# Kernel optimization log

Measured on AMD Instinct MI355X. Metric: run time of the kernel, lower is better.

## Reference

```python
import jax, jax.numpy as jnp
import numpy as np
import math

B, L, D = 4, 4096, 1024
M = 256  # num random features
EPS = 1e-06


def setup_inputs() -> dict:
    key = jax.random.key(0)
    kq, kk, kv, kp = jax.random.split(key, 4)
    Q = jax.random.normal(kq, (B, L, D), dtype=jnp.float32)
    K = jax.random.normal(kk, (B, L, D), dtype=jnp.float32)
    V = jax.random.normal(kv, (B, L, D), dtype=jnp.float32)
    # Gaussian random projection (ortho_features=False path): shape (num_features, d_model)
    projection = jax.random.normal(kp, (M, D), dtype=jnp.float32)
    return {"Q": Q, "K": K, "V": V, "projection": projection}


def reference(Q, K, V, projection):
    d_model = Q.shape[-1]
    m = projection.shape[0]
    inv_sqrt_d = 1.0 / math.sqrt(d_model)
    # random features: exp((x / sqrt(d)) @ P^T)
    rf_q = jnp.exp(jnp.einsum('bld,md->blm', Q * inv_sqrt_d, projection)) / math.sqrt(m)  # (B,L,M)
    rf_k = jnp.exp(jnp.einsum('bld,md->blm', K * inv_sqrt_d, projection))                 # (B,L,M)
    # linear attention: KV state and normalizer
    KV = jnp.einsum('blm,bld->bmd', rf_k, V)   # (B,M,D)
    Z = jnp.sum(rf_k, axis=1)                   # (B,M)
    out = jnp.einsum('blm,bmd->bld', rf_q, KV)  # (B,L,D)
    normalizer = jnp.einsum('blm,bm->bl', rf_q, Z) + EPS  # (B,L)
    return out / normalizer[..., None]
```

## Files before the change

kernel.cpp:

```cpp
#include <hip/hip_runtime.h>
#include <math.h>

#define NB 4
#define LL 4096
#define DD 1024
#define MM 256

typedef short s16x8 __attribute__((ext_vector_type(8)));
typedef short s16x4 __attribute__((ext_vector_type(4)));
typedef float fx4 __attribute__((ext_vector_type(4)));
typedef unsigned u32x2 __attribute__((ext_vector_type(2)));
typedef unsigned u32x4 __attribute__((ext_vector_type(4)));

__device__ __forceinline__ float b2f(short s) {
  union { unsigned u; float f; } v;
  v.u = ((unsigned)(unsigned short)s) << 16;
  return v.f;
}
__device__ __forceinline__ short f2b(float f) {
  union { float f; unsigned u; } v;
  v.f = f;
  unsigned r = (v.u + 0x7fffu + ((v.u >> 16) & 1u)) >> 16;
  return (short)(unsigned short)r;
}
__device__ __forceinline__ unsigned cvt2(float lo, float hi) {
  unsigned r;
  asm("v_cvt_pk_bf16_f32 %0, %1, %2" : "=v"(r) : "v"(lo), "v"(hi));
  return r;
}
__device__ __forceinline__ int keyf(int m) { return (m ^ (m >> 2)) & 3; }

typedef __attribute__((address_space(1))) const void* gas1_t;
typedef __attribute__((address_space(3))) void* las3_t;
#define GLL16(g, l) __builtin_amdgcn_global_load_lds((gas1_t)(const void*)(g), (las3_t)(void*)(l), 16, 0, 0)

__global__ __launch_bounds__(256) void k_cast(const float* __restrict__ in, short* __restrict__ out, int n4) {
  int i = blockIdx.x * 256 + threadIdx.x;
  if (i >= n4) return;
  float4 v = ((const float4*)in)[i];
  s16x4 s;
  s[0] = f2b(v.x); s[1] = f2b(v.y); s[2] = f2b(v.z); s[3] = f2b(v.w);
  ((s16x4*)out)[i] = s;
}

__global__ __launch_bounds__(256, 2) void k_qk(const float* __restrict__ Q, const float* __restrict__ K,
                                               const short* __restrict__ Pb,
                                               short* __restrict__ rfq, short* __restrict__ rfkT,
                                               float* __restrict__ Zz) {
  __shared__ short As[64 * 256];
  __shared__ short Bs[2][8192];
  int z = blockIdx.z, mode = z >> 2, b = z & 3;
  int l0 = blockIdx.x * 64;
  const float* X = mode ? K : Q;
  int tid = threadIdx.x, lane = tid & 63, w = tid >> 6;
  int m16 = lane & 15, kg = lane >> 4;

  int arow = tid >> 2, acol = (tid & 3) * 64;
  int akey = (arow & 7) << 4;
  char* Asb = (char*)As + arow * 512;

  fx4 acc[4][4] = {};

  for (int c = 0; c < 4; ++c) {
    if (c) __syncthreads();
    const float* Xc = X + ((size_t)b * LL + l0 + arow) * DD + c * 256 + acol;
    float4 pa[16];
    #pragma unroll
    for (int i = 0; i < 16; ++i) pa[i] = *(const float4*)(Xc + i * 4);
    #pragma unroll
    for (int j = 0; j < 4; ++j) {
      int fl = tid + j * 256, m = fl >> 2, ch = fl & 3;
      GLL16(Pb + (size_t)m * DD + c * 256 + (ch ^ keyf(m)) * 8, &Bs[0][fl * 8]);
    }
    #pragma unroll
    for (int i = 0; i < 8; ++i) {
      u32x4 v;
      v[0] = cvt2(pa[2 * i].x, pa[2 * i].y);
      v[1] = cvt2(pa[2 * i].z, pa[2 * i].w);
      v[2] = cvt2(pa[2 * i + 1].x, pa[2 * i + 1].y);
      v[3] = cvt2(pa[2 * i + 1].z, pa[2 * i + 1].w);
      int colb = (tid & 3) * 128 + i * 16;
      *(u32x4*)(Asb + (colb ^ akey)) = v;
    }
    __syncthreads();
    for (int s = 0; s < 8; ++s) {
      int buf = s & 1;
      if (s < 7) {
        #pragma unroll
        for (int j = 0; j < 4; ++j) {
          int fl = tid + j * 256, m = fl >> 2, ch = fl & 3;
          GLL16(Pb + (size_t)m * DD + c * 256 + (s + 1) * 32 + (ch ^ keyf(m)) * 8, &Bs[buf ^ 1][fl * 8]);
        }
      }
      s16x8 af[4], bf[4];
      int colb = s * 64 + kg * 16;
      #pragma unroll
      for (int mi = 0; mi < 4; ++mi) {
        int row = mi * 16 + m16;
        af[mi] = *(const s16x8*)((const char*)As + row * 512 + (colb ^ ((row & 7) << 4)));
      }
      #pragma unroll
      for (int ni = 0; ni < 4; ++ni) {
        int m = w * 64 + ni * 16 + m16;
        bf[ni] = *(const s16x8*)&Bs[buf][m * 32 + (kg ^ keyf(m)) * 8];
      }
      #pragma unroll
      for (int mi = 0; mi < 4; ++mi)
        #pragma unroll
        for (int ni = 0; ni < 4; ++ni)
          acc[mi][ni] = __builtin_amdgcn_mfma_f32_16x16x32_bf16(af[mi], bf[ni], acc[mi][ni], 0, 0, 0);
      if (s < 7) __syncthreads();
    }
  }

  if (mode == 0) {
    #pragma unroll
    for (int mi = 0; mi < 4; ++mi)
      #pragma unroll
      for (int ni = 0; ni < 4; ++ni) {
        int r0 = mi * 16 + (kg << 2);
        int c = w * 64 + ni * 16 + m16;
        #pragma unroll
        for (int u = 0; u < 4; ++u)
          rfq[((size_t)b * LL + l0 + r0 + u) * MM + c] = f2b(expf(acc[mi][ni][u] * 0.03125f) * 0.0625f);
      }
  } else {
    __syncthreads();
    short* T = (short*)Bs;
    float zp[4] = {0.f, 0.f, 0.f, 0.f};
    #pragma unroll
    for (int mi = 0; mi < 4; ++mi)
      #pragma unroll
      for (int ni = 0; ni < 4; ++ni) {
        int l = mi * 16 + (kg << 2);
        int m = w * 64 + ni * 16 + m16;
        int key = (m & 7) << 3;
        float e0 = expf(acc[mi][ni][0] * 0.03125f);
        float e1 = expf(acc[mi][ni][1] * 0.03125f);
        float e2 = expf(acc[mi][ni][2] * 0.03125f);
        float e3 = expf(acc[mi][ni][3] * 0.03125f);
        zp[ni] += e0 + e1 + e2 + e3;
        *(unsigned*)&T[m * 64 + (l ^ key)] = cvt2(e0, e1);
        *(unsigned*)&T[m * 64 + ((l ^ key) + 2)] = cvt2(e2, e3);
      }
    #pragma unroll
    for (int ni = 0; ni < 4; ++ni) {
      zp[ni] += __shfl_xor(zp[ni], 16);
      zp[ni] += __shfl_xor(zp[ni], 32);
    }
    if (kg == 0) {
      #pragma unroll
      for (int ni = 0; ni < 4; ++ni)
        atomicAdd(&Zz[b * MM + w * 64 + ni * 16 + m16], zp[ni]);
    }
    __syncthreads();
    int m = tid, mkey = (m & 7) << 3;
    short* dst = rfkT + ((size_t)b * MM + m) * LL + l0;
    #pragma unroll
    for (int j = 0; j < 8; ++j) {
      s16x8 v = *(const s16x8*)&T[m * 64 + ((j * 8) ^ mkey)];
      *(s16x8*)(dst + j * 8) = v;
    }
  }
}

__global__ __launch_bounds__(512) void k_kv(const float* __restrict__ V, const short* __restrict__ rfkT,
                                            float* __restrict__ KVp) {
  __shared__ float Vs[2][32 * 129];
  __shared__ short Ak[2][256 * 32];
  int d0 = blockIdx.x * 128, kc = blockIdx.y, b = blockIdx.z;
  int ls = kc * 512;
  int tid = threadIdx.x, lane = tid & 63, w = tid >> 6;
  int wm = w >> 1, wd = w & 1;
  int m16 = lane & 15, kg = lane >> 4;

  int vl = tid >> 4, vf = (tid & 15) * 8;
  const float* Vb = V + ((size_t)b * LL + ls + vl) * DD + d0 + vf;

  int am = tid >> 2, as = tid & 3;
  int acs = as ^ keyf(am);
  const short* AkS0 = rfkT + ((size_t)b * MM + am) * LL + ls + acs * 8;
  const short* AkS1 = rfkT + ((size_t)b * MM + am + 128) * LL + ls + acs * 8;

  fx4 acc[4][4] = {};
  float4 pv0, pv1;

  pv0 = *(const float4*)(Vb);
  pv1 = *(const float4*)(Vb + 4);
  GLL16(AkS0, &Ak[0][tid * 8]);
  GLL16(AkS1, &Ak[0][(tid + 512) * 8]);
  #pragma unroll
  for (int j = 0; j < 4; ++j) {
    Vs[0][vl * 129 + vf + j] = ((const float*)&pv0)[j];
    Vs[0][vl * 129 + vf + 4 + j] = ((const float*)&pv1)[j];
  }
  __syncthreads();

  for (int ch = 0; ch < 16; ++ch) {
    int cur = ch & 1, nxt = cur ^ 1;
    if (ch < 15) {
      int lo = (ch + 1) * 32;
      pv0 = *(const float4*)(Vb + (size_t)lo * DD);
      pv1 = *(const float4*)(Vb + (size_t)lo * DD + 4);
      GLL16(AkS0 + lo, &Ak[nxt][tid * 8]);
      GLL16(AkS1 + lo, &Ak[nxt][(tid + 512) * 8]);
    }
    s16x8 af[4];
    #pragma unroll
    for (int mi = 0; mi < 4; ++mi) {
      int m = wm * 64 + mi * 16 + m16;
      af[mi] = *(const s16x8*)&Ak[cur][m * 32 + ((kg ^ keyf(m)) * 8)];
    }
    #pragma unroll
    for (int ni = 0; ni < 4; ++ni) {
      int d = wd * 64 + ni * 16 + m16;
      const float* vs = &Vs[cur][kg * 8 * 129 + d];
      u32x4 bw;
      bw[0] = cvt2(vs[0], vs[129]);
      bw[1] = cvt2(vs[258], vs[387]);
      bw[2] = cvt2(vs[516], vs[645]);
      bw[3] = cvt2(vs[774], vs[903]);
      s16x8 bf = *(s16x8*)&bw;
      #pragma unroll
      for (int mi = 0; mi < 4; ++mi)
        acc[mi][ni] = __builtin_amdgcn_mfma_f32_16x16x32_bf16(af[mi], bf, acc[mi][ni], 0, 0, 0);
    }
    if (ch < 15) {
      #pragma unroll
      for (int j = 0; j < 4; ++j) {
        Vs[nxt][vl * 129 + vf + j] = ((const float*)&pv0)[j];
        Vs[nxt][vl * 129 + vf + 4 + j] = ((const float*)&pv1)[j];
      }
    }
    __syncthreads();
  }

  float* dst = KVp + (((size_t)kc * NB + b) * DD + d0) * MM;
  #pragma unroll
  for (int mi = 0; mi < 4; ++mi)
    #pragma unroll
    for (int ni = 0; ni < 4; ++ni) {
      int d = wd * 64 + ni * 16 + m16;
      int m = wm * 64 + mi * 16 + (kg << 2);
      *(float4*)(dst + (size_t)d * MM + m) = *(float4*)&acc[mi][ni];
    }
}

__global__ __launch_bounds__(256) void k_red(const float* __restrict__ KVp, float* __restrict__ KVTf) {
  int i = blockIdx.x * 256 + threadIdx.x;
  const float4* p = (const float4*)KVp;
  float4 s = p[i];
  #pragma unroll
  for (int k = 1; k < 8; ++k) {
    float4 v = p[i + k * 262144];
    s.x += v.x; s.y += v.y; s.z += v.z; s.w += v.w;
  }
  ((float4*)KVTf)[i] = s;
}

__global__ __launch_bounds__(512) void k_out(const short* __restrict__ rfq, const float* __restrict__ KVTf,
                                             const float* __restrict__ Zz, float* __restrict__ out) {
  __shared__ short Aq[2][8192];
  __shared__ short Bv[2][8192];
  __shared__ float zl[256];
  __shared__ float np[512];
  __shared__ float nf[128];
  int l0 = blockIdx.x * 128, d0 = blockIdx.y * 128, b = blockIdx.z;
  int tid = threadIdx.x, lane = tid & 63, w = tid >> 6;
  int wr = w >> 2, wc = w & 3;
  int brow = tid >> 2, bq = (tid & 3) * 16;
  int bkey = (brow & 7) << 3;
  const float* Kf = KVTf + ((size_t)b * DD + d0 + brow) * MM + bq;
  short* Bw0 = &Bv[0][brow * 64 + (bq ^ bkey)];
  short* Bw1 = &Bv[0][brow * 64 + ((bq + 8) ^ bkey)];
  const short* Ab = rfq + ((size_t)b * LL + l0) * MM;
  int f1 = tid + 512;
  int ar0 = tid >> 3, ac0 = tid & 7, ar1 = f1 >> 3, ac1 = f1 & 7;
  int nrow = tid & 127, nsub = tid >> 7;
  if (tid < 256) zl[tid] = Zz[b * MM + tid];
  fx4 acc[4][2] = {};
  float4 pb[4];
  float na = 0.f;

  #pragma unroll
  for (int i = 0; i < 4; ++i) pb[i] = *(const float4*)(Kf + i * 4);
  GLL16(Ab + (size_t)ar0 * MM + (ac0 ^ (ar0 & 7)) * 8, &Aq[0][tid * 8]);
  GLL16(Ab + (size_t)ar1 * MM + (ac1 ^ (ar1 & 7)) * 8, &Aq[0][f1 * 8]);
  {
    u32x2 v0, v1;
    v0[0] = cvt2(pb[0].x, pb[0].y); v0[1] = cvt2(pb[0].z, pb[0].w);
    v1[0] = cvt2(pb[1].x, pb[1].y); v1[1] = cvt2(pb[1].z, pb[1].w);
    *(u32x2*)Bw0 = v0;
    *(u32x2*)(Bw0 + 4) = v1;
    v0[0] = cvt2(pb[2].x, pb[2].y); v0[1] = cvt2(pb[2].z, pb[2].w);
    v1[0] = cvt2(pb[3].x, pb[3].y); v1[1] = cvt2(pb[3].z, pb[3].w);
    *(u32x2*)Bw1 = v0;
    *(u32x2*)(Bw1 + 4) = v1;
  }
  __syncthreads();

  for (int t = 0; t < 4; ++t) {
    int cur = t & 1, nxt = cur ^ 1;
    int m1 = ((t + 1) & 3) * 64;
    #pragma unroll
    for (int i = 0; i < 4; ++i) pb[i] = *(const float4*)(Kf + m1 + i * 4);
    GLL16(Ab + (size_t)ar0 * MM + m1 + (ac0 ^ (ar0 & 7)) * 8, &Aq[nxt][tid * 8]);
    GLL16(Ab + (size_t)ar1 * MM + m1 + (ac1 ^ (ar1 & 7)) * 8, &Aq[nxt][f1 * 8]);
    #pragma unroll
    for (int kk = 0; kk < 16; ++kk) {
      int k = nsub * 16 + kk;
      na += b2f(Aq[cur][nrow * 64 + (k ^ ((nrow & 7) << 3))]) * zl[t * 64 + k];
    }
    #pragma unroll
    for (int ks = 0; ks < 2; ++ks) {
      int kb = ks * 32 + (lane >> 4) * 8;
      s16x8 af[4], bf[2];
      #pragma unroll
      for (int mi = 0; mi < 4; ++mi) {
        int row = wr * 64 + mi * 16 + (lane & 15);
        af[mi] = *(const s16x8*)&Aq[cur][row * 64 + (kb ^ ((row & 7) << 3))];
      }
      #pragma unroll
      for (int ni = 0; ni < 2; ++ni) {
        int row = wc * 32 + ni * 16 + (lane & 15);
        bf[ni] = *(const s16x8*)&Bv[cur][row * 64 + (kb ^ ((row & 7) << 3))];
      }
      #pragma unroll
      for (int mi = 0; mi < 4; ++mi)
        #pragma unroll
        for (int ni = 0; ni < 2; ++ni)
          acc[mi][ni] = __builtin_amdgcn_mfma_f32_16x16x32_bf16(af[mi], bf[ni], acc[mi][ni], 0, 0, 0);
    }
    {
      u32x2 v0, v1;
      v0[0] = cvt2(pb[0].x, pb[0].y); v0[1] = cvt2(pb[0].z, pb[0].w);
      v1[0] = cvt2(pb[1].x, pb[1].y); v1[1] = cvt2(pb[1].z, pb[1].w);
      *(u32x2*)(Bw0 + nxt * 8192) = v0;
      *(u32x2*)(Bw0 + nxt * 8192 + 4) = v1;
      v0[0] = cvt2(pb[2].x, pb[2].y); v0[1] = cvt2(pb[2].z, pb[2].w);
      v1[0] = cvt2(pb[3].x, pb[3].y); v1[1] = cvt2(pb[3].z, pb[3].w);
      *(u32x2*)(Bw1 + nxt * 8192) = v0;
      *(u32x2*)(Bw1 + nxt * 8192 + 4) = v1;
    }
    __syncthreads();
  }
  np[tid] = na;
  __syncthreads();
  if (tid < 128) nf[tid] = np[tid] + np[tid + 128] + np[tid + 256] + np[tid + 384] + 1e-6f;
  __syncthreads();
  #pragma unroll
  for (int mi = 0; mi < 4; ++mi)
    #pragma unroll
    for (int ni = 0; ni < 2; ++ni) {
      int l = wr * 64 + mi * 16 + ((lane >> 4) << 2);
      int d = d0 + wc * 32 + ni * 16 + (lane & 15);
      #pragma unroll
      for (int u = 0; u < 4; ++u)
        out[((size_t)b * LL + l0 + l + u) * DD + d] = acc[mi][ni][u] / nf[l + u];
    }
}

extern "C" void kernel_launch(void* const* d_in, const int* in_sizes, int n_in,
                              void* d_out, int out_size, void* d_ws, size_t ws_size,
                              hipStream_t stream) {
  const float* Q = (const float*)d_in[0];
  const float* K = (const float*)d_in[1];
  const float* V = (const float*)d_in[2];
  const float* P = (const float*)d_in[3];
  float* out = (float*)d_out;
  char* ws = (char*)d_ws;

  short* Pb   = (short*)(ws + 0);
  float* Zz   = (float*)(ws + 524288);
  float* KVTf = (float*)(ws + 528384);
  short* rfq  = (short*)(ws + 4722688);
  short* rfkT = (short*)(ws + 13111296);
  float* KVp  = (float*)(ws + 21499904);

  k_cast<<<256, 256, 0, stream>>>(P, Pb, 65536);
  (void)hipMemsetAsync(Zz, 0, 4096, stream);
  k_qk<<<dim3(64, 1, 2 * NB), 256, 0, stream>>>(Q, K, Pb, rfq, rfkT, Zz);
  k_kv<<<dim3(8, 8, NB), 512, 0, stream>>>(V, rfkT, KVp);
  k_red<<<1024, 256, 0, stream>>>(KVp, KVTf);
  k_out<<<dim3(32, 8, NB), 512, 0, stream>>>(rfq, KVTf, Zz, out);
}
```

Measured before the change: 146.0 us.

## Stream fp32 Q/K tiles via async LDS loads in a unified double-buffered K loop

Replaces the per-256-column chunk staging of Q/K (register loads, bf16 conversion, store to LDS) with direct global-to-LDS async loads of fp32 tiles. These are double-buffered together with the projection tiles across a single 32-step K loop, using explicit vmcnt waits and raw barriers. The bf16 conversion moves to the fragment read from LDS. The aim is to overlap the activation load latency with MFMA work and drop the serial load-convert-store phase. In exchange it reads twice the LDS bytes for A, repeats the conversion in every wave, and relies on hand-tuned waitcnt counts for correctness.

```diff
diff --git a/kernel.cpp b/kernel.cpp
--- a/kernel.cpp
+++ b/kernel.cpp
@@ -47,7 +47,7 @@
                                                const short* __restrict__ Pb,
                                                short* __restrict__ rfq, short* __restrict__ rfkT,
                                                float* __restrict__ Zz) {
-  __shared__ short As[64 * 256];
+  __shared__ float As[2][2048];
   __shared__ short Bs[2][8192];
   int z = blockIdx.z, mode = z >> 2, b = z & 3;
   int l0 = blockIdx.x * 64;
@@ -55,62 +55,68 @@
   int tid = threadIdx.x, lane = tid & 63, w = tid >> 6;
   int m16 = lane & 15, kg = lane >> 4;
 
-  int arow = tid >> 2, acol = (tid & 3) * 64;
-  int akey = (arow & 7) << 4;
-  char* Asb = (char*)As + arow * 512;
+  int af0 = tid, af1 = tid + 256;
+  int ar0 = af0 >> 3, ag0 = af0 & 7, ar1 = af1 >> 3, ag1 = af1 & 7;
+  const float* aS0 = X + ((size_t)b * LL + l0 + ar0) * DD + (ag0 ^ (ar0 & 7)) * 4;
+  const float* aS1 = X + ((size_t)b * LL + l0 + ar1) * DD + (ag1 ^ (ar1 & 7)) * 4;
+  const short* bS[4];
+  #pragma unroll
+  for (int j = 0; j < 4; ++j) {
+    int fl = tid + j * 256, m = fl >> 2, ch = fl & 3;
+    bS[j] = Pb + (size_t)m * DD + (ch ^ keyf(m)) * 8;
+  }
 
   fx4 acc[4][4] = {};
 
-  for (int c = 0; c < 4; ++c) {
-    if (c) __syncthreads();
-    const float* Xc = X + ((size_t)b * LL + l0 + arow) * DD + c * 256 + acol;
-    float4 pa[16];
-    #pragma unroll
-    for (int i = 0; i < 16; ++i) pa[i] = *(const float4*)(Xc + i * 4);
-    #pragma unroll
-    for (int j = 0; j < 4; ++j) {
-      int fl = tid + j * 256, m = fl >> 2, ch = fl & 3;
-      GLL16(Pb + (size_t)m * DD + c * 256 + (ch ^ keyf(m)) * 8, &Bs[0][fl * 8]);
-    }
-    #pragma unroll
-    for (int i = 0; i < 8; ++i) {
-      u32x4 v;
-      v[0] = cvt2(pa[2 * i].x, pa[2 * i].y);
-      v[1] = cvt2(pa[2 * i].z, pa[2 * i].w);
-      v[2] = cvt2(pa[2 * i + 1].x, pa[2 * i + 1].y);
-      v[3] = cvt2(pa[2 * i + 1].z, pa[2 * i + 1].w);
-      int colb = (tid & 3) * 128 + i * 16;
-      *(u32x4*)(Asb + (colb ^ akey)) = v;
-    }
-    __syncthreads();
-    for (int s = 0; s < 8; ++s) {
-      int buf = s & 1;
-      if (s < 7) {
-        #pragma unroll
-        for (int j = 0; j < 4; ++j) {
-          int fl = tid + j * 256, m = fl >> 2, ch = fl & 3;
-          GLL16(Pb + (size_t)m * DD + c * 256 + (s + 1) * 32 + (ch ^ keyf(m)) * 8, &Bs[buf ^ 1][fl * 8]);
-        }
-      }
-      s16x8 af[4], bf[4];
-      int colb = s * 64 + kg * 16;
-      #pragma unroll
-      for (int mi = 0; mi < 4; ++mi) {
-        int row = mi * 16 + m16;
-        af[mi] = *(const s16x8*)((const char*)As + row * 512 + (colb ^ ((row & 7) << 4)));
-      }
-      #pragma unroll
-      for (int ni = 0; ni < 4; ++ni) {
-        int m = w * 64 + ni * 16 + m16;
-        bf[ni] = *(const s16x8*)&Bs[buf][m * 32 + (kg ^ keyf(m)) * 8];
-      }
-      #pragma unroll
-      for (int mi = 0; mi < 4; ++mi)
-        #pragma unroll
-        for (int ni = 0; ni < 4; ++ni)
-          acc[mi][ni] = __builtin_amdgcn_mfma_f32_16x16x32_bf16(af[mi], bf[ni], acc[mi][ni], 0, 0, 0);
-      if (s < 7) __syncthreads();
-    }
+  {
+    GLL16(aS0, &As[0][af0 * 4]);
+    GLL16(aS1, &As[0][af1 * 4]);
+    #pragma unroll
+    for (int j = 0; j < 4; ++j) GLL16(bS[j], &Bs[0][(tid + j * 256) * 8]);
+  }
+
+  for (int t = 0; t < 32; ++t) {
+    int cur = t & 1, nxt = cur ^ 1;
+    if (t < 31) {
+      int ko = (t + 1) * 32;
+      GLL16(aS0 + ko, &As[nxt][af0 * 4]);
+      GLL16(aS1 + ko, &As[nxt][af1 * 4]);
+      #pragma unroll
+      for (int j = 0; j < 4; ++j) GLL16(bS[j] + ko, &Bs[nxt][(tid + j * 256) * 8]);
+    }
+    __builtin_amdgcn_sched_barrier(0);
+    if (t < 31) asm volatile("s_waitcnt vmcnt(6)" ::: "memory");
+    else        asm volatile("s_waitcnt vmcnt(0)" ::: "memory");
+    __builtin_amdgcn_sched_barrier(0);
+    __builtin_amdgcn_s_barrier();
+    __builtin_amdgcn_sched_barrier(0);
+
+    s16x8 af[4], bf[4];
+    #pragma unroll
+    for (int mi = 0; mi < 4; ++mi) {
+      int r = mi * 16 + m16, rk = r & 7;
+      const float* pr = &As[cur][r * 32];
+      fx4 a0 = *(const fx4*)(pr + ((2 * kg) ^ rk) * 4);
+      fx4 a1 = *(const fx4*)(pr + ((2 * kg + 1) ^ rk) * 4);
+      u32x4 aw;
+      aw[0] = cvt2(a0[0], a0[1]); aw[1] = cvt2(a0[2], a0[3]);
+      aw[2] = cvt2(a1[0], a1[1]); aw[3] = cvt2(a1[2], a1[3]);
+      af[mi] = *(s16x8*)&aw;
+    }
+    #pragma unroll
+    for (int ni = 0; ni < 4; ++ni) {
+      int m = w * 64 + ni * 16 + m16;
+      bf[ni] = *(const s16x8*)&Bs[cur][m * 32 + (kg ^ keyf(m)) * 8];
+    }
+    #pragma unroll
+    for (int mi = 0; mi < 4; ++mi)
+      #pragma unroll
+      for (int ni = 0; ni < 4; ++ni)
+        acc[mi][ni] = __builtin_amdgcn_mfma_f32_16x16x32_bf16(af[mi], bf[ni], acc[mi][ni], 0, 0, 0);
+
+    __builtin_amdgcn_sched_barrier(0);
+    __builtin_amdgcn_s_barrier();
+    __builtin_amdgcn_sched_barrier(0);
   }
 
   if (mode == 0) {
```

After: 141.2 us. 3.3% less time.
